# Optimization experiments

Measured on AMD Instinct MI355X. Metric: run time of the kernel, lower is better.

Reference implementation:

```python
import jax, jax.numpy as jnp
import numpy as np

DIM = 512
N = 131072


def _linear_params(key, dim):
    # torch nn.Linear default init: U(-1/sqrt(in), 1/sqrt(in)) for W and b
    kw, kb = jax.random.split(key)
    bound = 1.0 / np.sqrt(dim)
    W = jax.random.uniform(kw, (dim, dim), jnp.float32, -bound, bound)
    b = jax.random.uniform(kb, (dim,), jnp.float32, -bound, bound)
    return W, b


def setup_inputs() -> dict:
    key = jax.random.key(0)
    ks = jax.random.split(key, 8)
    x = jax.random.normal(ks[0], (N, DIM), jnp.float32)
    h = jax.random.normal(ks[1], (N, DIM), jnp.float32)
    W_rx, b_rx = _linear_params(ks[2], DIM)
    W_rh, b_rh = _linear_params(ks[3], DIM)
    W_zx, b_zx = _linear_params(ks[4], DIM)
    W_zh, b_zh = _linear_params(ks[5], DIM)
    W_nx, b_nx = _linear_params(ks[6], DIM)
    W_nh, b_nh = _linear_params(ks[7], DIM)
    return {
        "x": x, "h": h,
        "W_rx": W_rx, "b_rx": b_rx, "W_rh": W_rh, "b_rh": b_rh,
        "W_zx": W_zx, "b_zx": b_zx, "W_zh": W_zh, "b_zh": b_zh,
        "W_nx": W_nx, "b_nx": b_nx, "W_nh": W_nh, "b_nh": b_nh,
    }


def reference(x, h, W_rx, b_rx, W_rh, b_rh, W_zx, b_zx, W_zh, b_zh,
              W_nx, b_nx, W_nh, b_nh):
    # torch Linear: y = x @ W.T + b  (W stored [out, in])
    r = jax.nn.sigmoid(x @ W_rx.T + b_rx + h @ W_rh.T + b_rh)
    z = jax.nn.sigmoid(x @ W_zx.T + b_zx + h @ W_zh.T + b_zh)
    n = jnp.tanh(x @ W_nx.T + b_nx + (r * h) @ W_nh.T + b_nh)
    return (1.0 - z) * n + z * h
```

## Files before the change

kernel.cpp:

```cpp
#include <hip/hip_runtime.h>

#define DIM 512
#define NROWS 131072

typedef __attribute__((ext_vector_type(8))) __bf16 bf16x8;
typedef __attribute__((ext_vector_type(4))) float f32x4;

__device__ __forceinline__ unsigned short f2bf(float f) {
  unsigned u = __builtin_bit_cast(unsigned, f);
  return (unsigned short)((u + 0x7FFFu + ((u >> 16) & 1u)) >> 16);
}
__device__ __forceinline__ float bf2f(unsigned short u) {
  return __builtin_bit_cast(float, (unsigned)u << 16);
}

__device__ __forceinline__ f32x4 mfma16(bf16x8 a, bf16x8 b, f32x4 c) {
  return __builtin_amdgcn_mfma_f32_16x16x32_bf16(a, b, c, 0, 0, 0);
}

__device__ __forceinline__ float sigmoid_fast(float v) {
  return 1.0f / (1.0f + __expf(-v));
}
__device__ __forceinline__ float tanh_fast(float v) {
  float e = __expf(2.0f * v);
  return 1.0f - 2.0f / (e + 1.0f);
}

__device__ __forceinline__ void gl2lds(const void* g, void* l) {
  __builtin_amdgcn_global_load_lds(
      (const __attribute__((address_space(1))) unsigned int*)g,
      (__attribute__((address_space(3))) unsigned int*)l, 16, 0, 0);
}

__global__ void prepack_weights(const float* __restrict__ W0, const float* __restrict__ W1,
                                const float* __restrict__ W2, const float* __restrict__ W3,
                                const float* __restrict__ W4, const float* __restrict__ W5,
                                unsigned short* __restrict__ out) {
  int idx = blockIdx.x * 256 + threadIdx.x;
  int e = idx & 7;
  int l = (idx >> 3) & 63;
  int c = (idx >> 9) & 31;
  int f = (idx >> 14) & 15;
  int g = idx >> 18;
  const float* W = (g == 0) ? W0 : (g == 1) ? W1 : (g == 2) ? W2
                 : (g == 3) ? W3 : (g == 4) ? W4 : W5;
  int row = c * 16 + (l & 15);
  int kk  = f * 32 + ((l >> 4) << 3) + e;
  out[idx] = f2bf(W[row * DIM + kk]);
}

__global__ void prep_x(const float* __restrict__ x, unsigned short* __restrict__ xb) {
  size_t i = (size_t)(blockIdx.x * 256 + threadIdx.x) * 8;
  float4 a0 = *(const float4*)(x + i);
  float4 a1 = *(const float4*)(x + i + 4);
  union { unsigned short us[8]; uint4 v; } p;
  p.us[0] = f2bf(a0.x); p.us[1] = f2bf(a0.y); p.us[2] = f2bf(a0.z); p.us[3] = f2bf(a0.w);
  p.us[4] = f2bf(a1.x); p.us[5] = f2bf(a1.y); p.us[6] = f2bf(a1.z); p.us[7] = f2bf(a1.w);
  *(uint4*)(xb + i) = p.v;
}

#define BOFF 65536
#define XOFF 131072
#define LDS_BYTES 147456

__global__ __launch_bounds__(512, 1)
void gru_fused(const float* __restrict__ x, const float* __restrict__ h,
               const unsigned short* __restrict__ xb,
               const unsigned char* __restrict__ WB,
               const float* __restrict__ b_rx, const float* __restrict__ b_rh,
               const float* __restrict__ b_zx, const float* __restrict__ b_zh,
               const float* __restrict__ b_nx, const float* __restrict__ b_nh,
               float* __restrict__ out) {
  __shared__ __align__(1024) unsigned char lds[LDS_BYTES];

  const int tid  = threadIdx.x;
  const int lane = tid & 63;
  const int w    = tid >> 6;
  const int cfg0 = w * 4;
  const int row0 = blockIdx.x * 64;
  const int lr   = lane & 15;
  const int lk   = lane >> 4;

  auto stageB = [&](int g, int f, int dst) {
    const unsigned char* src = WB + (size_t)(g * 16 + f) * 32768;
#pragma unroll
    for (int it = 0; it < 4; ++it) {
      int o = (it * 512 + tid) * 16;
      gl2lds(src + o, &lds[dst + o]);
    }
  };
  auto stageXpair = [&](int p) {
    int fh = tid >> 8, rf = (tid >> 6) & 3, l = tid & 63;
    const unsigned short* src = xb + (size_t)(row0 + rf * 16 + (l & 15)) * DIM
                                + p * 64 + fh * 32 + (l >> 4) * 8;
    gl2lds(src, &lds[XOFF + (p & 1) * 8192 + tid * 16]);
  };
  auto gateStage = [&](int abase, int bbase, f32x4 (&A)[4][4]) {
    bf16x8 af[4], bfr[4];
#pragma unroll
    for (int rf = 0; rf < 4; ++rf)
      af[rf] = *(const bf16x8*)&lds[abase + rf * 1024 + lane * 16];
#pragma unroll
    for (int cf = 0; cf < 4; ++cf)
      bfr[cf] = *(const bf16x8*)&lds[bbase + (cfg0 + cf) * 1024 + lane * 16];
#pragma unroll
    for (int rf = 0; rf < 4; ++rf)
#pragma unroll
      for (int cf = 0; cf < 4; ++cf)
        A[rf][cf] = mfma16(af[rf], bfr[cf], A[rf][cf]);
  };

  f32x4 accR[4][4] = {}, accZ[4][4] = {};

#pragma unroll
  for (int it = 0; it < 16; ++it) {
    int i = tid + it * 512;
    int row = i >> 7;
    int k = (i & 127) * 4;
    float4 hv4 = *(const float4*)(h + (size_t)(row0 + row) * DIM + k);
    union { unsigned short us[4]; uint2 v; } p;
    p.us[0] = f2bf(hv4.x); p.us[1] = f2bf(hv4.y);
    p.us[2] = f2bf(hv4.z); p.us[3] = f2bf(hv4.w);
    *(uint2*)&lds[(k >> 5) * 4096 + (row >> 4) * 1024
                  + (((k >> 3) & 3) * 16 + (row & 15)) * 16 + (k & 4) * 2] = p.v;
  }
  stageXpair(0);
  stageB(0, 0, BOFF);
  __syncthreads();

#pragma unroll 1
  for (int f = 0; f < 16; ++f) {
    const int xo = XOFF + ((f >> 1) & 1) * 8192 + (f & 1) * 4096;
    const int ho = f * 4096;
    stageB(1, f, BOFF + 32768);
    if (f & 1) {
      int p1 = (f >> 1) + 1; if (p1 > 7) p1 = 7;
      stageXpair(p1);
      asm volatile("s_waitcnt vmcnt(5)" ::: "memory");
    } else {
      asm volatile("s_waitcnt vmcnt(4)" ::: "memory");
    }
    __builtin_amdgcn_s_barrier();
    gateStage(xo, BOFF, accR);
    __builtin_amdgcn_s_barrier();
    stageB(2, f, BOFF);
    asm volatile("s_waitcnt vmcnt(4)" ::: "memory");
    __builtin_amdgcn_s_barrier();
    gateStage(xo, BOFF + 32768, accZ);
    __builtin_amdgcn_s_barrier();
    stageB(3, f, BOFF + 32768);
    asm volatile("s_waitcnt vmcnt(4)" ::: "memory");
    __builtin_amdgcn_s_barrier();
    gateStage(ho, BOFF, accR);
    __builtin_amdgcn_s_barrier();
    if (f < 15) {
      stageB(0, f + 1, BOFF);
      asm volatile("s_waitcnt vmcnt(4)" ::: "memory");
    } else {
      asm volatile("s_waitcnt vmcnt(0)" ::: "memory");
    }
    __builtin_amdgcn_s_barrier();
    gateStage(ho, BOFF + 32768, accZ);
    __builtin_amdgcn_s_barrier();
  }

#pragma unroll
  for (int cf = 0; cf < 4; ++cf) {
    const int col  = (cfg0 + cf) * 16 + lr;
    const float bs = b_rx[col] + b_rh[col];
    const int fcol  = col >> 5;
    const int l2b   = ((col >> 3) & 3) * 16;
    const int ebyte = (col & 7) * 2;
#pragma unroll
    for (int rf = 0; rf < 4; ++rf) {
#pragma unroll
      for (int j = 0; j < 4; ++j) {
        const int rsub = lk * 4 + j;
        unsigned short hu = *(const unsigned short*)
            &lds[fcol * 4096 + rf * 1024 + (l2b + rsub) * 16 + ebyte];
        float rv = sigmoid_fast(accR[rf][cf][j] + bs);
        *(unsigned short*)
            &lds[BOFF + fcol * 4096 + rf * 1024 + (l2b + rsub) * 16 + ebyte]
            = f2bf(rv * bf2f(hu));
      }
    }
  }
  __syncthreads();

  f32x4 accN[4][4] = {};
  stageXpair(0);
  stageB(4, 0, 0);
#pragma unroll 1
  for (int f = 0; f < 16; ++f) {
    const int xo = XOFF + ((f >> 1) & 1) * 8192 + (f & 1) * 4096;
    stageB(5, f, 32768);
    if (f & 1) {
      int p1 = (f >> 1) + 1; if (p1 > 7) p1 = 7;
      stageXpair(p1);
      asm volatile("s_waitcnt vmcnt(5)" ::: "memory");
    } else {
      asm volatile("s_waitcnt vmcnt(4)" ::: "memory");
    }
    __builtin_amdgcn_s_barrier();
    gateStage(xo, 0, accN);
    __builtin_amdgcn_s_barrier();
    if (f < 15) {
      stageB(4, f + 1, 0);
      asm volatile("s_waitcnt vmcnt(4)" ::: "memory");
    } else {
      asm volatile("s_waitcnt vmcnt(0)" ::: "memory");
    }
    __builtin_amdgcn_s_barrier();
    gateStage(BOFF + f * 4096, 32768, accN);
    __builtin_amdgcn_s_barrier();
  }

#pragma unroll
  for (int cf = 0; cf < 4; ++cf) {
    const int col  = (cfg0 + cf) * 16 + lr;
    const float bn = b_nx[col] + b_nh[col];
    const float bz = b_zx[col] + b_zh[col];
#pragma unroll
    for (int rf = 0; rf < 4; ++rf) {
#pragma unroll
      for (int j = 0; j < 4; ++j) {
        const int row = rf * 16 + lk * 4 + j;
        const size_t off = (size_t)(row0 + row) * DIM + col;
        float hv = h[off];
        float nv = tanh_fast(accN[rf][cf][j] + bn);
        float zv = sigmoid_fast(accZ[rf][cf][j] + bz);
        out[off] = (1.0f - zv) * nv + zv * hv;
      }
    }
  }
}

extern "C" void kernel_launch(void* const* d_in, const int* in_sizes, int n_in,
                              void* d_out, int out_size, void* d_ws, size_t ws_size,
                              hipStream_t stream) {
  const float* x    = (const float*)d_in[0];
  const float* h    = (const float*)d_in[1];
  const float* W_rx = (const float*)d_in[2];
  const float* b_rx = (const float*)d_in[3];
  const float* W_rh = (const float*)d_in[4];
  const float* b_rh = (const float*)d_in[5];
  const float* W_zx = (const float*)d_in[6];
  const float* b_zx = (const float*)d_in[7];
  const float* W_zh = (const float*)d_in[8];
  const float* b_zh = (const float*)d_in[9];
  const float* W_nx = (const float*)d_in[10];
  const float* b_nx = (const float*)d_in[11];
  const float* W_nh = (const float*)d_in[12];
  const float* b_nh = (const float*)d_in[13];

  unsigned char* ws = (unsigned char*)d_ws;
  unsigned short* wpack = (unsigned short*)ws;
  unsigned short* xb    = (unsigned short*)(ws + (4ull << 20));

  prepack_weights<<<6144, 256, 0, stream>>>(W_rx, W_zx, W_rh, W_zh, W_nx, W_nh, wpack);
  prep_x<<<32768, 256, 0, stream>>>(x, xb);
  gru_fused<<<NROWS / 64, 512, 0, stream>>>(x, h, xb, (const unsigned char*)wpack,
                                            b_rx, b_rh, b_zx, b_zh, b_nx, b_nh,
                                            (float*)d_out);
}
```

Baseline: 671.1 us.

## Prepack h to bf16 panels and software-pipeline LDS operand reads in GRU kernel

Adds a prep_h kernel that converts h to bf16 in the MFMA fragment layout, so the fused kernel can load its h tile straight into LDS with async copies instead of converting fp32 in-kernel. The main loops are restructured to prefetch the next A fragments into registers while the current MFMAs run, and manual vmcnt waits with split barriers are replaced by __syncthreads. MFMA bursts are also wrapped in s_setprio. In exchange there is an extra launch and an extra round trip of h through global memory, and the waitcnt handling now relies on what __syncthreads implies.

```diff
diff --git a/kernel.cpp b/kernel.cpp
--- a/kernel.cpp
+++ b/kernel.cpp
@@ -59,6 +59,25 @@
   *(uint4*)(xb + i) = p.v;
 }
 
+__global__ void prep_h(const float* __restrict__ h, unsigned short* __restrict__ hfb) {
+  size_t idx  = (size_t)(blockIdx.x * 256 + threadIdx.x);
+  size_t base = idx * 8;
+  size_t panel = base >> 15;
+  int rem  = (int)(base & 32767);
+  int f    = rem >> 11;
+  int rf   = (rem >> 9) & 3;
+  int lane = (rem >> 3) & 63;
+  int row  = (int)panel * 64 + rf * 16 + (lane & 15);
+  int k    = f * 32 + (lane >> 4) * 8;
+  const float* src = h + (size_t)row * DIM + k;
+  float4 a0 = *(const float4*)src;
+  float4 a1 = *(const float4*)(src + 4);
+  union { unsigned short us[8]; uint4 v; } p;
+  p.us[0] = f2bf(a0.x); p.us[1] = f2bf(a0.y); p.us[2] = f2bf(a0.z); p.us[3] = f2bf(a0.w);
+  p.us[4] = f2bf(a1.x); p.us[5] = f2bf(a1.y); p.us[6] = f2bf(a1.z); p.us[7] = f2bf(a1.w);
+  *(uint4*)(hfb + base) = p.v;
+}
+
 #define BOFF 65536
 #define XOFF 131072
 #define LDS_BYTES 147456
@@ -66,6 +85,7 @@
 __global__ __launch_bounds__(512, 1)
 void gru_fused(const float* __restrict__ x, const float* __restrict__ h,
                const unsigned short* __restrict__ xb,
+               const unsigned short* __restrict__ hfb,
                const unsigned char* __restrict__ WB,
                const float* __restrict__ b_rx, const float* __restrict__ b_rh,
                const float* __restrict__ b_zx, const float* __restrict__ b_zh,
@@ -95,73 +115,81 @@
                                 + p * 64 + fh * 32 + (l >> 4) * 8;
     gl2lds(src, &lds[XOFF + (p & 1) * 8192 + tid * 16]);
   };
-  auto gateStage = [&](int abase, int bbase, f32x4 (&A)[4][4]) {
-    bf16x8 af[4], bfr[4];
+  auto readA = [&](int abase, bf16x8 (&af)[4]) {
 #pragma unroll
     for (int rf = 0; rf < 4; ++rf)
       af[rf] = *(const bf16x8*)&lds[abase + rf * 1024 + lane * 16];
+  };
+  auto readB = [&](int bbase, bf16x8 (&bfr)[4]) {
 #pragma unroll
     for (int cf = 0; cf < 4; ++cf)
       bfr[cf] = *(const bf16x8*)&lds[bbase + (cfg0 + cf) * 1024 + lane * 16];
+  };
+  auto domfma = [&](bf16x8 (&af)[4], bf16x8 (&bfr)[4], f32x4 (&A)[4][4]) {
+    __builtin_amdgcn_s_setprio(1);
 #pragma unroll
     for (int rf = 0; rf < 4; ++rf)
 #pragma unroll
       for (int cf = 0; cf < 4; ++cf)
         A[rf][cf] = mfma16(af[rf], bfr[cf], A[rf][cf]);
+    __builtin_amdgcn_s_setprio(0);
   };
 
   f32x4 accR[4][4] = {}, accZ[4][4] = {};
-
-#pragma unroll
-  for (int it = 0; it < 16; ++it) {
-    int i = tid + it * 512;
-    int row = i >> 7;
-    int k = (i & 127) * 4;
-    float4 hv4 = *(const float4*)(h + (size_t)(row0 + row) * DIM + k);
-    union { unsigned short us[4]; uint2 v; } p;
-    p.us[0] = f2bf(hv4.x); p.us[1] = f2bf(hv4.y);
-    p.us[2] = f2bf(hv4.z); p.us[3] = f2bf(hv4.w);
-    *(uint2*)&lds[(k >> 5) * 4096 + (row >> 4) * 1024
-                  + (((k >> 3) & 3) * 16 + (row & 15)) * 16 + (k & 4) * 2] = p.v;
-  }
+  bf16x8 afx[4], afh[4], bfr[4];
+
+  stageB(0, 0, BOFF);
   stageXpair(0);
-  stageB(0, 0, BOFF);
+  if (hfb) {
+    const unsigned char* src = (const unsigned char*)(hfb + (size_t)blockIdx.x * 32768);
+#pragma unroll
+    for (int it = 0; it < 8; ++it) {
+      int o = (it * 512 + tid) * 16;
+      gl2lds(src + o, &lds[o]);
+    }
+  } else {
+#pragma unroll
+    for (int it = 0; it < 16; ++it) {
+      int i = tid + it * 512;
+      int row = i >> 7;
+      int k = (i & 127) * 4;
+      float4 hv4 = *(const float4*)(h + (size_t)(row0 + row) * DIM + k);
+      union { unsigned short us[4]; uint2 v; } p;
+      p.us[0] = f2bf(hv4.x); p.us[1] = f2bf(hv4.y);
+      p.us[2] = f2bf(hv4.z); p.us[3] = f2bf(hv4.w);
+      *(uint2*)&lds[(k >> 5) * 4096 + (row >> 4) * 1024
+                    + (((k >> 3) & 3) * 16 + (row & 15)) * 16 + (k & 4) * 2] = p.v;
+    }
+  }
   __syncthreads();
+  readA(XOFF, afx);
 
 #pragma unroll 1
   for (int f = 0; f < 16; ++f) {
-    const int xo = XOFF + ((f >> 1) & 1) * 8192 + (f & 1) * 4096;
-    const int ho = f * 4096;
     stageB(1, f, BOFF + 32768);
-    if (f & 1) {
-      int p1 = (f >> 1) + 1; if (p1 > 7) p1 = 7;
-      stageXpair(p1);
-      asm volatile("s_waitcnt vmcnt(5)" ::: "memory");
-    } else {
-      asm volatile("s_waitcnt vmcnt(4)" ::: "memory");
-    }
-    __builtin_amdgcn_s_barrier();
-    gateStage(xo, BOFF, accR);
-    __builtin_amdgcn_s_barrier();
+    readB(BOFF, bfr);
+    domfma(afx, bfr, accR);
+    __syncthreads();
     stageB(2, f, BOFF);
-    asm volatile("s_waitcnt vmcnt(4)" ::: "memory");
-    __builtin_amdgcn_s_barrier();
-    gateStage(xo, BOFF + 32768, accZ);
-    __builtin_amdgcn_s_barrier();
+    readB(BOFF + 32768, bfr);
+    readA(f * 4096, afh);
+    domfma(afx, bfr, accZ);
+    __syncthreads();
     stageB(3, f, BOFF + 32768);
-    asm volatile("s_waitcnt vmcnt(4)" ::: "memory");
-    __builtin_amdgcn_s_barrier();
-    gateStage(ho, BOFF, accR);
-    __builtin_amdgcn_s_barrier();
+    readB(BOFF, bfr);
+    domfma(afh, bfr, accR);
+    __syncthreads();
     if (f < 15) {
       stageB(0, f + 1, BOFF);
-      asm volatile("s_waitcnt vmcnt(4)" ::: "memory");
-    } else {
-      asm volatile("s_waitcnt vmcnt(0)" ::: "memory");
-    }
-    __builtin_amdgcn_s_barrier();
-    gateStage(ho, BOFF + 32768, accZ);
-    __builtin_amdgcn_s_barrier();
+      if (!(f & 1) && f < 14) stageXpair((f >> 1) + 1);
+    }
+    readB(BOFF + 32768, bfr);
+    if (f < 15) {
+      int fn = f + 1;
+      readA(XOFF + ((fn >> 1) & 1) * 8192 + (fn & 1) * 4096, afx);
+    }
+    domfma(afh, bfr, accZ);
+    __syncthreads();
   }
 
 #pragma unroll
@@ -188,31 +216,28 @@
   __syncthreads();
 
   f32x4 accN[4][4] = {};
+  stageB(4, 0, 0);
   stageXpair(0);
-  stageB(4, 0, 0);
+  __syncthreads();
+  readA(XOFF, afx);
 #pragma unroll 1
   for (int f = 0; f < 16; ++f) {
-    const int xo = XOFF + ((f >> 1) & 1) * 8192 + (f & 1) * 4096;
     stageB(5, f, 32768);
-    if (f & 1) {
-      int p1 = (f >> 1) + 1; if (p1 > 7) p1 = 7;
-      stageXpair(p1);
-      asm volatile("s_waitcnt vmcnt(5)" ::: "memory");
-    } else {
-      asm volatile("s_waitcnt vmcnt(4)" ::: "memory");
-    }
-    __builtin_amdgcn_s_barrier();
-    gateStage(xo, 0, accN);
-    __builtin_amdgcn_s_barrier();
+    readB(0, bfr);
+    readA(BOFF + f * 4096, afh);
+    domfma(afx, bfr, accN);
+    __syncthreads();
     if (f < 15) {
       stageB(4, f + 1, 0);
-      asm volatile("s_waitcnt vmcnt(4)" ::: "memory");
-    } else {
-      asm volatile("s_waitcnt vmcnt(0)" ::: "memory");
-    }
-    __builtin_amdgcn_s_barrier();
-    gateStage(BOFF + f * 4096, 32768, accN);
-    __builtin_amdgcn_s_barrier();
+      if (!(f & 1) && f < 14) stageXpair((f >> 1) + 1);
+    }
+    readB(32768, bfr);
+    if (f < 15) {
+      int fn = f + 1;
+      readA(XOFF + ((fn >> 1) & 1) * 8192 + (fn & 1) * 4096, afx);
+    }
+    domfma(afh, bfr, accN);
+    __syncthreads();
   }
 
 #pragma unroll
@@ -256,10 +281,16 @@
   unsigned char* ws = (unsigned char*)d_ws;
   unsigned short* wpack = (unsigned short*)ws;
   unsigned short* xb    = (unsigned short*)(ws + (4ull << 20));
+  const size_t hfb_off  = (4ull << 20) + (size_t)NROWS * DIM * 2;
+  const size_t need_h   = hfb_off + (size_t)NROWS * DIM * 2;
+  unsigned short* hfb   = (ws_size >= need_h) ? (unsigned short*)(ws + hfb_off)
+                                              : (unsigned short*)nullptr;
 
   prepack_weights<<<6144, 256, 0, stream>>>(W_rx, W_zx, W_rh, W_zh, W_nx, W_nh, wpack);
   prep_x<<<32768, 256, 0, stream>>>(x, xb);
-  gru_fused<<<NROWS / 64, 512, 0, stream>>>(x, h, xb, (const unsigned char*)wpack,
+  if (hfb) prep_h<<<32768, 256, 0, stream>>>(h, hfb);
+  gru_fused<<<NROWS / 64, 512, 0, stream>>>(x, h, xb, hfb,
+                                            (const unsigned char*)wpack,
                                             b_rx, b_rh, b_zx, b_zh, b_nx, b_nh,
                                             (float*)d_out);
 }
```

After: 835.6 us. 24.5% more time.

## Triple-buffer weight tiles, load x fragments directly to registers, one barrier per stage

Applied to the files above, without the earlier changes.

Replaces the double-buffered weight staging, which needed two barriers per MFMA stage, with a three-slot ring buffer, so each stage needs one barrier and the next tile's prefetch overlaps the current stage's MFMAs. The x operand fragments are now loaded from global memory straight into registers one step ahead, instead of being staged through LDS. The r*h product is written back in place over h in LDS, and MFMA blocks are wrapped in s_setprio. The intent is to cut barrier stalls and LDS traffic, at the cost of more registers and tighter vmcnt bookkeeping that is easy to get wrong.

```diff
diff --git a/kernel.cpp b/kernel.cpp
--- a/kernel.cpp
+++ b/kernel.cpp
@@ -13,11 +13,9 @@
 __device__ __forceinline__ float bf2f(unsigned short u) {
   return __builtin_bit_cast(float, (unsigned)u << 16);
 }
-
 __device__ __forceinline__ f32x4 mfma16(bf16x8 a, bf16x8 b, f32x4 c) {
   return __builtin_amdgcn_mfma_f32_16x16x32_bf16(a, b, c, 0, 0, 0);
 }
-
 __device__ __forceinline__ float sigmoid_fast(float v) {
   return 1.0f / (1.0f + __expf(-v));
 }
@@ -25,7 +23,6 @@
   float e = __expf(2.0f * v);
   return 1.0f - 2.0f / (e + 1.0f);
 }
-
 __device__ __forceinline__ void gl2lds(const void* g, void* l) {
   __builtin_amdgcn_global_load_lds(
       (const __attribute__((address_space(1))) unsigned int*)g,
@@ -60,11 +57,10 @@
 }
 
 #define BOFF 65536
-#define XOFF 131072
-#define LDS_BYTES 147456
+#define LDS_BYTES 163840
 
 __global__ __launch_bounds__(512, 1)
-void gru_fused(const float* __restrict__ x, const float* __restrict__ h,
+void gru_fused(const float* __restrict__ h,
                const unsigned short* __restrict__ xb,
                const unsigned char* __restrict__ WB,
                const float* __restrict__ b_rx, const float* __restrict__ b_rh,
@@ -81,37 +77,48 @@
   const int lr   = lane & 15;
   const int lk   = lane >> 4;
 
-  auto stageB = [&](int g, int f, int dst) {
+  auto stageB = [&](int g, int f, int buf) {
     const unsigned char* src = WB + (size_t)(g * 16 + f) * 32768;
 #pragma unroll
     for (int it = 0; it < 4; ++it) {
       int o = (it * 512 + tid) * 16;
-      gl2lds(src + o, &lds[dst + o]);
+      gl2lds(src + o, &lds[BOFF + buf * 32768 + o]);
     }
   };
-  auto stageXpair = [&](int p) {
-    int fh = tid >> 8, rf = (tid >> 6) & 3, l = tid & 63;
-    const unsigned short* src = xb + (size_t)(row0 + rf * 16 + (l & 15)) * DIM
-                                + p * 64 + fh * 32 + (l >> 4) * 8;
-    gl2lds(src, &lds[XOFF + (p & 1) * 8192 + tid * 16]);
-  };
-  auto gateStage = [&](int abase, int bbase, f32x4 (&A)[4][4]) {
-    bf16x8 af[4], bfr[4];
+  auto loadXA = [&](int f, bf16x8 (&a)[4]) {
 #pragma unroll
     for (int rf = 0; rf < 4; ++rf)
-      af[rf] = *(const bf16x8*)&lds[abase + rf * 1024 + lane * 16];
+      a[rf] = *(const bf16x8*)(xb + (size_t)(row0 + rf * 16 + lr) * DIM
+                               + f * 32 + lk * 8);
+  };
+  auto readAh = [&](int f, bf16x8 (&a)[4]) {
+#pragma unroll
+    for (int rf = 0; rf < 4; ++rf)
+      a[rf] = *(const bf16x8*)&lds[f * 4096 + rf * 1024 + lane * 16];
+  };
+  auto readB = [&](int buf, bf16x8 (&b)[4]) {
 #pragma unroll
     for (int cf = 0; cf < 4; ++cf)
-      bfr[cf] = *(const bf16x8*)&lds[bbase + (cfg0 + cf) * 1024 + lane * 16];
-#pragma unroll
-    for (int rf = 0; rf < 4; ++rf)
-#pragma unroll
-      for (int cf = 0; cf < 4; ++cf)
-        A[rf][cf] = mfma16(af[rf], bfr[cf], A[rf][cf]);
-  };
-
-  f32x4 accR[4][4] = {}, accZ[4][4] = {};
-
+      b[cf] = *(const bf16x8*)&lds[BOFF + buf * 32768 + (cfg0 + cf) * 1024
+                                   + lane * 16];
+  };
+
+#define WIN(A, B, ACC)                                                         \
+  do {                                                                         \
+    __builtin_amdgcn_s_setprio(1);                                             \
+    _Pragma("unroll")                                                          \
+    for (int rf_ = 0; rf_ < 4; ++rf_)                                          \
+      _Pragma("unroll")                                                        \
+      for (int cf_ = 0; cf_ < 4; ++cf_)                                        \
+        ACC[rf_][cf_] = mfma16(A[rf_], B[cf_], ACC[rf_][cf_]);                 \
+    __builtin_amdgcn_s_setprio(0);                                             \
+  } while (0)
+
+  bf16x8 afx[4], afxN[4], afh[4], bfr[4];
+
+  loadXA(0, afx);
+  stageB(0, 0, 0);
+  stageB(1, 0, 1);
 #pragma unroll
   for (int it = 0; it < 16; ++it) {
     int i = tid + it * 512;
@@ -124,95 +131,97 @@
     *(uint2*)&lds[(k >> 5) * 4096 + (row >> 4) * 1024
                   + (((k >> 3) & 3) * 16 + (row & 15)) * 16 + (k & 4) * 2] = p.v;
   }
-  stageXpair(0);
-  stageB(0, 0, BOFF);
   __syncthreads();
 
+  f32x4 accR[4][4] = {}, accZ[4][4] = {};
+  int c0 = 0;
 #pragma unroll 1
   for (int f = 0; f < 16; ++f) {
-    const int xo = XOFF + ((f >> 1) & 1) * 8192 + (f & 1) * 4096;
-    const int ho = f * 4096;
-    stageB(1, f, BOFF + 32768);
-    if (f & 1) {
-      int p1 = (f >> 1) + 1; if (p1 > 7) p1 = 7;
-      stageXpair(p1);
-      asm volatile("s_waitcnt vmcnt(5)" ::: "memory");
-    } else {
-      asm volatile("s_waitcnt vmcnt(4)" ::: "memory");
-    }
-    __builtin_amdgcn_s_barrier();
-    gateStage(xo, BOFF, accR);
-    __builtin_amdgcn_s_barrier();
-    stageB(2, f, BOFF);
-    asm volatile("s_waitcnt vmcnt(4)" ::: "memory");
-    __builtin_amdgcn_s_barrier();
-    gateStage(xo, BOFF + 32768, accZ);
-    __builtin_amdgcn_s_barrier();
-    stageB(3, f, BOFF + 32768);
-    asm volatile("s_waitcnt vmcnt(4)" ::: "memory");
-    __builtin_amdgcn_s_barrier();
-    gateStage(ho, BOFF, accR);
-    __builtin_amdgcn_s_barrier();
-    if (f < 15) {
-      stageB(0, f + 1, BOFF);
-      asm volatile("s_waitcnt vmcnt(4)" ::: "memory");
-    } else {
-      asm volatile("s_waitcnt vmcnt(0)" ::: "memory");
-    }
-    __builtin_amdgcn_s_barrier();
-    gateStage(ho, BOFF + 32768, accZ);
-    __builtin_amdgcn_s_barrier();
-  }
-
+    const int c1 = (c0 == 2) ? 0 : c0 + 1;
+    const int c2 = (c1 == 2) ? 0 : c1 + 1;
+    asm volatile("s_waitcnt vmcnt(4)" ::: "memory");
+    __builtin_amdgcn_s_barrier();
+    stageB(2, f, c2);
+    readB(c0, bfr);
+    WIN(afx, bfr, accR);
+    asm volatile("s_waitcnt vmcnt(4)" ::: "memory");
+    __builtin_amdgcn_s_barrier();
+    stageB(3, f, c0);
+    readB(c1, bfr);
+    WIN(afx, bfr, accZ);
+    asm volatile("s_waitcnt vmcnt(4)" ::: "memory");
+    __builtin_amdgcn_s_barrier();
+    if (f < 15) { loadXA(f + 1, afxN); stageB(0, f + 1, c1); }
+    else        { loadXA(0, afxN);     stageB(4, 0, c1); }
+    readAh(f, afh);
+    readB(c2, bfr);
+    WIN(afh, bfr, accR);
+    asm volatile("s_waitcnt vmcnt(8)" ::: "memory");
+    __builtin_amdgcn_s_barrier();
+    stageB((f < 15) ? 1 : 5, (f < 15) ? f + 1 : 0, c2);
+    readB(c0, bfr);
+    WIN(afh, bfr, accZ);
+#pragma unroll
+    for (int i2 = 0; i2 < 4; ++i2) afx[i2] = afxN[i2];
+    c0 = c1;
+  }
+
+  __builtin_amdgcn_s_barrier();
 #pragma unroll
   for (int cf = 0; cf < 4; ++cf) {
     const int col  = (cfg0 + cf) * 16 + lr;
     const float bs = b_rx[col] + b_rh[col];
-    const int fcol  = col >> 5;
-    const int l2b   = ((col >> 3) & 3) * 16;
-    const int ebyte = (col & 7) * 2;
+    const int fI  = col >> 5;
+    const int l2b = ((col >> 3) & 3) * 16;
+    const int eb  = (col & 7) * 2;
 #pragma unroll
     for (int rf = 0; rf < 4; ++rf) {
 #pragma unroll
       for (int j = 0; j < 4; ++j) {
         const int rsub = lk * 4 + j;
-        unsigned short hu = *(const unsigned short*)
-            &lds[fcol * 4096 + rf * 1024 + (l2b + rsub) * 16 + ebyte];
+        const int addr = fI * 4096 + rf * 1024 + (l2b + rsub) * 16 + eb;
+        unsigned short hu = *(const unsigned short*)&lds[addr];
         float rv = sigmoid_fast(accR[rf][cf][j] + bs);
-        *(unsigned short*)
-            &lds[BOFF + fcol * 4096 + rf * 1024 + (l2b + rsub) * 16 + ebyte]
-            = f2bf(rv * bf2f(hu));
+        *(unsigned short*)&lds[addr] = f2bf(rv * bf2f(hu));
       }
     }
   }
-  __syncthreads();
+  asm volatile("s_waitcnt lgkmcnt(0)" ::: "memory");
 
   f32x4 accN[4][4] = {};
-  stageXpair(0);
-  stageB(4, 0, 0);
+  int d0 = 1;
 #pragma unroll 1
-  for (int f = 0; f < 16; ++f) {
-    const int xo = XOFF + ((f >> 1) & 1) * 8192 + (f & 1) * 4096;
-    stageB(5, f, 32768);
-    if (f & 1) {
-      int p1 = (f >> 1) + 1; if (p1 > 7) p1 = 7;
-      stageXpair(p1);
-      asm volatile("s_waitcnt vmcnt(5)" ::: "memory");
-    } else {
-      asm volatile("s_waitcnt vmcnt(4)" ::: "memory");
-    }
-    __builtin_amdgcn_s_barrier();
-    gateStage(xo, 0, accN);
-    __builtin_amdgcn_s_barrier();
-    if (f < 15) {
-      stageB(4, f + 1, 0);
-      asm volatile("s_waitcnt vmcnt(4)" ::: "memory");
-    } else {
-      asm volatile("s_waitcnt vmcnt(0)" ::: "memory");
-    }
-    __builtin_amdgcn_s_barrier();
-    gateStage(BOFF + f * 4096, 32768, accN);
-    __builtin_amdgcn_s_barrier();
+  for (int f = 0; f < 15; ++f) {
+    const int d1 = (d0 == 2) ? 0 : d0 + 1;
+    const int e0 = (d1 == 2) ? 0 : d1 + 1;
+    const int e1 = (e0 == 2) ? 0 : e0 + 1;
+    asm volatile("s_waitcnt vmcnt(4)" ::: "memory");
+    __builtin_amdgcn_s_barrier();
+    loadXA(f + 1, afxN);
+    stageB(4, f + 1, e0);
+    readB(d0, bfr);
+    WIN(afx, bfr, accN);
+    asm volatile("s_waitcnt vmcnt(8)" ::: "memory");
+    __builtin_amdgcn_s_barrier();
+    stageB(5, f + 1, e1);
+    readAh(f, afh);
+    readB(d1, bfr);
+    WIN(afh, bfr, accN);
+#pragma unroll
+    for (int i2 = 0; i2 < 4; ++i2) afx[i2] = afxN[i2];
+    d0 = e0;
+  }
+  {
+    asm volatile("s_waitcnt vmcnt(4)" ::: "memory");
+    __builtin_amdgcn_s_barrier();
+    readB(d0, bfr);
+    WIN(afx, bfr, accN);
+    const int d1 = (d0 == 2) ? 0 : d0 + 1;
+    asm volatile("s_waitcnt vmcnt(0)" ::: "memory");
+    __builtin_amdgcn_s_barrier();
+    readAh(15, afh);
+    readB(d1, bfr);
+    WIN(afh, bfr, accN);
   }
 
 #pragma unroll
@@ -233,6 +242,7 @@
       }
     }
   }
+#undef WIN
 }
 
 extern "C" void kernel_launch(void* const* d_in, const int* in_sizes, int n_in,
@@ -259,7 +269,7 @@
 
   prepack_weights<<<6144, 256, 0, stream>>>(W_rx, W_zx, W_rh, W_zh, W_nx, W_nh, wpack);
   prep_x<<<32768, 256, 0, stream>>>(x, xb);
-  gru_fused<<<NROWS / 64, 512, 0, stream>>>(x, h, xb, (const unsigned char*)wpack,
+  gru_fused<<<NROWS / 64, 512, 0, stream>>>(h, xb, (const unsigned char*)wpack,
                                             b_rx, b_rh, b_zx, b_zh, b_nx, b_nh,
                                             (float*)d_out);
 }
```

After: 837.3 us. 1.25x slower.

## Split GRU into three gate sweeps with bf16 h staging and 2-block occupancy

Applied to the files above, without the earlier changes.

Adds a new kernel that computes the z, r and n gates in three separate K sweeps. Each sweep uses 256-thread blocks with a 64x512 output tile, and the A fragments (x, h and r*h in bf16) are read straight from global memory rather than staged in LDS. LDS use drops to 64KB so two blocks can share a CU. The kernel also swizzles the block order and raises MFMA priority. The cost is an extra conversion pass for h, plus global round-trips of r*h and z through workspace buffers. The old fused kernel is kept as a fallback for when the workspace is too small.

```diff
diff --git a/kernel.cpp b/kernel.cpp
--- a/kernel.cpp
+++ b/kernel.cpp
@@ -13,11 +13,9 @@
 __device__ __forceinline__ float bf2f(unsigned short u) {
   return __builtin_bit_cast(float, (unsigned)u << 16);
 }
-
 __device__ __forceinline__ f32x4 mfma16(bf16x8 a, bf16x8 b, f32x4 c) {
   return __builtin_amdgcn_mfma_f32_16x16x32_bf16(a, b, c, 0, 0, 0);
 }
-
 __device__ __forceinline__ float sigmoid_fast(float v) {
   return 1.0f / (1.0f + __expf(-v));
 }
@@ -25,7 +23,6 @@
   float e = __expf(2.0f * v);
   return 1.0f - 2.0f / (e + 1.0f);
 }
-
 __device__ __forceinline__ void gl2lds(const void* g, void* l) {
   __builtin_amdgcn_global_load_lds(
       (const __attribute__((address_space(1))) unsigned int*)g,
@@ -49,29 +46,169 @@
   out[idx] = f2bf(W[row * DIM + kk]);
 }
 
-__global__ void prep_x(const float* __restrict__ x, unsigned short* __restrict__ xb) {
+__global__ void prep_bf16(const float* __restrict__ in, unsigned short* __restrict__ ob) {
   size_t i = (size_t)(blockIdx.x * 256 + threadIdx.x) * 8;
-  float4 a0 = *(const float4*)(x + i);
-  float4 a1 = *(const float4*)(x + i + 4);
+  float4 a0 = *(const float4*)(in + i);
+  float4 a1 = *(const float4*)(in + i + 4);
   union { unsigned short us[8]; uint4 v; } p;
   p.us[0] = f2bf(a0.x); p.us[1] = f2bf(a0.y); p.us[2] = f2bf(a0.z); p.us[3] = f2bf(a0.w);
   p.us[4] = f2bf(a1.x); p.us[5] = f2bf(a1.y); p.us[6] = f2bf(a1.z); p.us[7] = f2bf(a1.w);
-  *(uint4*)(xb + i) = p.v;
-}
-
-#define BOFF 65536
-#define XOFF 131072
-#define LDS_BYTES 147456
+  *(uint4*)(ob + i) = p.v;
+}
+
+__global__ __launch_bounds__(256, 2)
+void gru_3sweep(const float* __restrict__ h,
+                const unsigned short* __restrict__ xb,
+                const unsigned short* __restrict__ hb,
+                unsigned short* __restrict__ rhb,
+                unsigned short* __restrict__ zb,
+                const unsigned char* __restrict__ WB,
+                const float* __restrict__ b_rx, const float* __restrict__ b_rh,
+                const float* __restrict__ b_zx, const float* __restrict__ b_zh,
+                const float* __restrict__ b_nx, const float* __restrict__ b_nh,
+                float* __restrict__ out) {
+  __shared__ __align__(1024) unsigned char lds[65536];
+
+  const int tid  = threadIdx.x;
+  const int lane = tid & 63;
+  const int w    = tid >> 6;
+  const int bid  = blockIdx.x;
+  const int swz  = (bid & 7) * 256 + (bid >> 3);
+  const int row0 = swz * 64;
+  const int lr   = lane & 15;
+  const int lk   = lane >> 4;
+
+  f32x4 acc[4][8];
+  bf16x8 af[4], bfr[8];
+
+  auto stageB = [&](int g, int f, int buf) {
+    const unsigned char* src = WB + (size_t)(g * 16 + f) * 32768;
+#pragma unroll
+    for (int it = 0; it < 8; ++it) {
+      int o = (it * 256 + tid) * 16;
+      gl2lds(src + o, &lds[buf * 32768 + o]);
+    }
+  };
+  auto loadAf = [&](const unsigned short* base, int f) {
+#pragma unroll
+    for (int rf = 0; rf < 4; ++rf)
+      af[rf] = *(const bf16x8*)(base + (size_t)(row0 + rf * 16 + lr) * DIM
+                                + f * 32 + lk * 8);
+  };
+  auto readB = [&](int buf) {
+#pragma unroll
+    for (int cf = 0; cf < 8; ++cf)
+      bfr[cf] = *(const bf16x8*)&lds[buf * 32768 + (w * 8 + cf) * 1024 + lane * 16];
+  };
+
+#define MFMA32()                                                               \
+  do {                                                                         \
+    __builtin_amdgcn_s_setprio(1);                                             \
+    _Pragma("unroll")                                                          \
+    for (int rf_ = 0; rf_ < 4; ++rf_)                                          \
+      _Pragma("unroll")                                                        \
+      for (int cf_ = 0; cf_ < 8; ++cf_)                                        \
+        acc[rf_][cf_] = mfma16(af[rf_], bfr[cf_], acc[rf_][cf_]);              \
+    __builtin_amdgcn_s_setprio(0);                                             \
+  } while (0)
+
+#define SWEEP(GX, GH, HSRC, NEXTG, HAVE_NEXT)                                  \
+  {                                                                            \
+    _Pragma("unroll")                                                          \
+    for (int rf_ = 0; rf_ < 4; ++rf_)                                          \
+      _Pragma("unroll")                                                        \
+      for (int cf_ = 0; cf_ < 8; ++cf_)                                        \
+        acc[rf_][cf_] = (f32x4){0.f, 0.f, 0.f, 0.f};                           \
+    _Pragma("unroll 1")                                                        \
+    for (int f = 0; f < 16; ++f) {                                             \
+                         \
+      loadAf(xb, f);                                                           \
+      stageB((GH), f, 1);                                                      \
+      asm volatile("s_waitcnt vmcnt(8)" ::: "memory");                         \
+      __builtin_amdgcn_s_barrier();                                            \
+      readB(0);                                                                \
+      MFMA32();                                                                \
+      __builtin_amdgcn_s_barrier();                                            \
+            \
+      loadAf((HSRC), f);                                                       \
+      if (f < 15)            stageB((GX), f + 1, 0);                           \
+      else if (HAVE_NEXT)    stageB((NEXTG), 0, 0);                            \
+      if (f < 15 || HAVE_NEXT)                                                 \
+        asm volatile("s_waitcnt vmcnt(8)" ::: "memory");                       \
+      else                                                                     \
+        asm volatile("s_waitcnt vmcnt(0)" ::: "memory");                       \
+      __builtin_amdgcn_s_barrier();                                            \
+      readB(1);                                                                \
+      MFMA32();                                                                \
+      __builtin_amdgcn_s_barrier();                                            \
+    }                                                                          \
+  }
+
+  stageB(1, 0, 0);
+
+  SWEEP(1, 3, hb, 0, true);
+#pragma unroll
+  for (int cf = 0; cf < 8; ++cf) {
+    const int col = (w * 8 + cf) * 16 + lr;
+    const float bz = b_zx[col] + b_zh[col];
+#pragma unroll
+    for (int rf = 0; rf < 4; ++rf)
+#pragma unroll
+      for (int j = 0; j < 4; ++j) {
+        const size_t off = (size_t)(row0 + rf * 16 + lk * 4 + j) * DIM + col;
+        const float zv = sigmoid_fast(acc[rf][cf][j] + bz);
+        if (zb) zb[off] = f2bf(zv); else out[off] = zv;
+      }
+  }
+
+  SWEEP(0, 2, hb, 4, true);
+#pragma unroll
+  for (int cf = 0; cf < 8; ++cf) {
+    const int col = (w * 8 + cf) * 16 + lr;
+    const float bs = b_rx[col] + b_rh[col];
+#pragma unroll
+    for (int rf = 0; rf < 4; ++rf)
+#pragma unroll
+      for (int j = 0; j < 4; ++j) {
+        const size_t off = (size_t)(row0 + rf * 16 + lk * 4 + j) * DIM + col;
+        const float rv = sigmoid_fast(acc[rf][cf][j] + bs);
+        rhb[off] = f2bf(rv * bf2f(hb[off]));
+      }
+  }
+  __syncthreads();
+
+  SWEEP(4, 5, rhb, 0, false);
+#pragma unroll
+  for (int cf = 0; cf < 8; ++cf) {
+    const int col = (w * 8 + cf) * 16 + lr;
+    const float bn = b_nx[col] + b_nh[col];
+#pragma unroll
+    for (int rf = 0; rf < 4; ++rf)
+#pragma unroll
+      for (int j = 0; j < 4; ++j) {
+        const size_t off = (size_t)(row0 + rf * 16 + lk * 4 + j) * DIM + col;
+        const float nv = tanh_fast(acc[rf][cf][j] + bn);
+        const float zv = zb ? bf2f(zb[off]) : out[off];
+        out[off] = (1.0f - zv) * nv + zv * h[off];
+      }
+  }
+#undef SWEEP
+#undef MFMA32
+}
+
+#define R5_BOFF 65536
+#define R5_XOFF 131072
+#define R5_LDS  147456
 
 __global__ __launch_bounds__(512, 1)
-void gru_fused(const float* __restrict__ x, const float* __restrict__ h,
-               const unsigned short* __restrict__ xb,
-               const unsigned char* __restrict__ WB,
-               const float* __restrict__ b_rx, const float* __restrict__ b_rh,
-               const float* __restrict__ b_zx, const float* __restrict__ b_zh,
-               const float* __restrict__ b_nx, const float* __restrict__ b_nh,
-               float* __restrict__ out) {
-  __shared__ __align__(1024) unsigned char lds[LDS_BYTES];
+void gru_fused_r5(const float* __restrict__ h,
+                  const unsigned short* __restrict__ xb,
+                  const unsigned char* __restrict__ WB,
+                  const float* __restrict__ b_rx, const float* __restrict__ b_rh,
+                  const float* __restrict__ b_zx, const float* __restrict__ b_zh,
+                  const float* __restrict__ b_nx, const float* __restrict__ b_nh,
+                  float* __restrict__ out) {
+  __shared__ __align__(1024) unsigned char lds[R5_LDS];
 
   const int tid  = threadIdx.x;
   const int lane = tid & 63;
@@ -93,7 +230,7 @@
     int fh = tid >> 8, rf = (tid >> 6) & 3, l = tid & 63;
     const unsigned short* src = xb + (size_t)(row0 + rf * 16 + (l & 15)) * DIM
                                 + p * 64 + fh * 32 + (l >> 4) * 8;
-    gl2lds(src, &lds[XOFF + (p & 1) * 8192 + tid * 16]);
+    gl2lds(src, &lds[R5_XOFF + (p & 1) * 8192 + tid * 16]);
   };
   auto gateStage = [&](int abase, int bbase, f32x4 (&A)[4][4]) {
     bf16x8 af[4], bfr[4];
@@ -125,14 +262,14 @@
                   + (((k >> 3) & 3) * 16 + (row & 15)) * 16 + (k & 4) * 2] = p.v;
   }
   stageXpair(0);
-  stageB(0, 0, BOFF);
+  stageB(0, 0, R5_BOFF);
   __syncthreads();
 
 #pragma unroll 1
   for (int f = 0; f < 16; ++f) {
-    const int xo = XOFF + ((f >> 1) & 1) * 8192 + (f & 1) * 4096;
+    const int xo = R5_XOFF + ((f >> 1) & 1) * 8192 + (f & 1) * 4096;
     const int ho = f * 4096;
-    stageB(1, f, BOFF + 32768);
+    stageB(1, f, R5_BOFF + 32768);
     if (f & 1) {
       int p1 = (f >> 1) + 1; if (p1 > 7) p1 = 7;
       stageXpair(p1);
@@ -141,26 +278,26 @@
       asm volatile("s_waitcnt vmcnt(4)" ::: "memory");
     }
     __builtin_amdgcn_s_barrier();
-    gateStage(xo, BOFF, accR);
-    __builtin_amdgcn_s_barrier();
-    stageB(2, f, BOFF);
+    gateStage(xo, R5_BOFF, accR);
+    __builtin_amdgcn_s_barrier();
+    stageB(2, f, R5_BOFF);
     asm volatile("s_waitcnt vmcnt(4)" ::: "memory");
     __builtin_amdgcn_s_barrier();
-    gateStage(xo, BOFF + 32768, accZ);
-    __builtin_amdgcn_s_barrier();
-    stageB(3, f, BOFF + 32768);
+    gateStage(xo, R5_BOFF + 32768, accZ);
+    __builtin_amdgcn_s_barrier();
+    stageB(3, f, R5_BOFF + 32768);
     asm volatile("s_waitcnt vmcnt(4)" ::: "memory");
     __builtin_amdgcn_s_barrier();
-    gateStage(ho, BOFF, accR);
+    gateStage(ho, R5_BOFF, accR);
     __builtin_amdgcn_s_barrier();
     if (f < 15) {
-      stageB(0, f + 1, BOFF);
+      stageB(0, f + 1, R5_BOFF);
       asm volatile("s_waitcnt vmcnt(4)" ::: "memory");
     } else {
       asm volatile("s_waitcnt vmcnt(0)" ::: "memory");
     }
     __builtin_amdgcn_s_barrier();
-    gateStage(ho, BOFF + 32768, accZ);
+    gateStage(ho, R5_BOFF + 32768, accZ);
     __builtin_amdgcn_s_barrier();
   }
 
@@ -180,7 +317,7 @@
             &lds[fcol * 4096 + rf * 1024 + (l2b + rsub) * 16 + ebyte];
         float rv = sigmoid_fast(accR[rf][cf][j] + bs);
         *(unsigned short*)
-            &lds[BOFF + fcol * 4096 + rf * 1024 + (l2b + rsub) * 16 + ebyte]
+            &lds[R5_BOFF + fcol * 4096 + rf * 1024 + (l2b + rsub) * 16 + ebyte]
             = f2bf(rv * bf2f(hu));
       }
     }
@@ -192,7 +329,7 @@
   stageB(4, 0, 0);
 #pragma unroll 1
   for (int f = 0; f < 16; ++f) {
-    const int xo = XOFF + ((f >> 1) & 1) * 8192 + (f & 1) * 4096;
+    const int xo = R5_XOFF + ((f >> 1) & 1) * 8192 + (f & 1) * 4096;
     stageB(5, f, 32768);
     if (f & 1) {
       int p1 = (f >> 1) + 1; if (p1 > 7) p1 = 7;
@@ -211,7 +348,7 @@
       asm volatile("s_waitcnt vmcnt(0)" ::: "memory");
     }
     __builtin_amdgcn_s_barrier();
-    gateStage(BOFF + f * 4096, 32768, accN);
+    gateStage(R5_BOFF + f * 4096, 32768, accN);
     __builtin_amdgcn_s_barrier();
   }
 
@@ -255,11 +392,34 @@
 
   unsigned char* ws = (unsigned char*)d_ws;
   unsigned short* wpack = (unsigned short*)ws;
-  unsigned short* xb    = (unsigned short*)(ws + (4ull << 20));
+  const size_t SEG = (size_t)NROWS * DIM * 2;
+  const size_t xb_off  = 4ull << 20;
+  const size_t hb_off  = xb_off + SEG;
+  const size_t rhb_off = hb_off + SEG;
+  const size_t zb_off  = rhb_off + SEG;
+  const size_t need_main = zb_off;
+  const size_t need_zb   = zb_off + SEG;
 
   prepack_weights<<<6144, 256, 0, stream>>>(W_rx, W_zx, W_rh, W_zh, W_nx, W_nh, wpack);
-  prep_x<<<32768, 256, 0, stream>>>(x, xb);
-  gru_fused<<<NROWS / 64, 512, 0, stream>>>(x, h, xb, (const unsigned char*)wpack,
-                                            b_rx, b_rh, b_zx, b_zh, b_nx, b_nh,
-                                            (float*)d_out);
-}
+
+  if (ws_size >= need_main) {
+    unsigned short* xb  = (unsigned short*)(ws + xb_off);
+    unsigned short* hb  = (unsigned short*)(ws + hb_off);
+    unsigned short* rhb = (unsigned short*)(ws + rhb_off);
+    unsigned short* zb  = (ws_size >= need_zb) ? (unsigned short*)(ws + zb_off)
+                                               : (unsigned short*)nullptr;
+    prep_bf16<<<32768, 256, 0, stream>>>(x, xb);
+    prep_bf16<<<32768, 256, 0, stream>>>(h, hb);
+    gru_3sweep<<<NROWS / 64, 256, 0, stream>>>(h, xb, hb, rhb, zb,
+                                               (const unsigned char*)wpack,
+                                               b_rx, b_rh, b_zx, b_zh, b_nx, b_nh,
+                                               (float*)d_out);
+  } else {
+    unsigned short* xb = (unsigned short*)(ws + xb_off);
+    prep_bf16<<<32768, 256, 0, stream>>>(x, xb);
+    gru_fused_r5<<<NROWS / 64, 512, 0, stream>>>(h, xb,
+                                                 (const unsigned char*)wpack,
+                                                 b_rx, b_rh, b_zx, b_zh, b_nx, b_nh,
+                                                 (float*)d_out);
+  }
+}
```

After: 1.557 ms. 132% more time.
